# Kernel optimization log

Measured on AMD Instinct MI355X. Metric: run time of the kernel, lower is better.

## Reference

```python
import jax, jax.numpy as jnp
import numpy as np

D = 256      # dim
H = 8        # num_heads
HD = D // H  # head dim
P = 256      # patch_size
B = 4        # num clouds
L = 32768    # points per cloud (divisible by P)
N = B * L
MLP = int(D * 2.0)
PEH = max(32, D // 4)
EPS = 1e-5


def setup_inputs() -> dict:
    key = jax.random.key(0)
    ks = jax.random.split(key, 20)
    s = 0.02
    w = lambda k, shp: jax.random.normal(k, shp, jnp.float32) * s
    inp = {
        "feats": jax.random.normal(ks[0], (N, D), jnp.float32),
        "coord": jax.random.uniform(ks[1], (N, 3), jnp.float32),
        "lengths": jnp.full((B,), L, jnp.int32),
        # CoordPositionalEncoding: Linear(3,PEH) -> ReLU -> Linear(PEH,D)
        "pe_w1": w(ks[2], (3, PEH)), "pe_b1": jnp.zeros((PEH,), jnp.float32),
        "pe_w2": w(ks[3], (PEH, D)), "pe_b2": jnp.zeros((D,), jnp.float32),
        "pre_g": jnp.ones((D,), jnp.float32), "pre_b": jnp.zeros((D,), jnp.float32),
        # block: norm1 + MHA + norm2 + MLP
        "n1_g": jnp.ones((D,), jnp.float32), "n1_b": jnp.zeros((D,), jnp.float32),
        "wqkv": w(ks[4], (D, 3 * D)), "bqkv": jnp.zeros((3 * D,), jnp.float32),
        "wo": w(ks[5], (D, D)), "bo": jnp.zeros((D,), jnp.float32),
        "n2_g": jnp.ones((D,), jnp.float32), "n2_b": jnp.zeros((D,), jnp.float32),
        "m_w1": w(ks[6], (D, MLP)), "m_b1": jnp.zeros((MLP,), jnp.float32),
        "m_w2": w(ks[7], (MLP, D)), "m_b2": jnp.zeros((D,), jnp.float32),
        # global_gate: Linear(2D,D)->ReLU->Linear(D,D)->Sigmoid
        "gg_w1": w(ks[8], (2 * D, D)), "gg_b1": jnp.zeros((D,), jnp.float32),
        "gg_w2": w(ks[9], (D, D)), "gg_b2": jnp.zeros((D,), jnp.float32),
        # fuse: Linear(2D,D)->ReLU->Linear(D,D)
        "f_w1": w(ks[10], (2 * D, D)), "f_b1": jnp.zeros((D,), jnp.float32),
        "f_w2": w(ks[11], (D, D)), "f_b2": jnp.zeros((D,), jnp.float32),
    }
    return inp


def _ln(x, g, b):
    m = x.mean(-1, keepdims=True)
    v = jnp.mean((x - m) ** 2, -1, keepdims=True)
    return (x - m) * jax.lax.rsqrt(v + EPS) * g + b


def _sgca(feats, coord, lengths,
          pe_w1, pe_b1, pe_w2, pe_b2, pre_g, pre_b,
          n1_g, n1_b, wqkv, bqkv, wo, bo, n2_g, n2_b,
          m_w1, m_b1, m_w2, m_b2,
          gg_w1, gg_b1, gg_w2, gg_b2, f_w1, f_b1, f_w2, f_b2):
    Bn = lengths.shape[0]
    Ln = feats.shape[0] // Bn  # equal-length clouds

    def cloud(f, c):  # f: [L, D], c: [L, 3]
        # positional encoding (per-cloud centered / max-abs scaled coords)
        cc = c - c.mean(0, keepdims=True)
        scale = jnp.clip(jnp.abs(cc).max(0, keepdims=True), 1e-6)
        pe = jax.nn.relu((cc / scale) @ pe_w1 + pe_b1) @ pe_w2 + pe_b2
        x = _ln(f + pe, pre_g, pre_b)
        # serialization order from min-max normalized coords
        cn = c - c.min(0, keepdims=True)
        cn = cn / jnp.clip(cn.max(0, keepdims=True), 1e-6)
        key = cn[:, 0] + 2.17 * cn[:, 1] + 3.31 * cn[:, 2]
        order = jnp.argsort(key)
        xs = x[order].reshape(-1, P, D)  # [NP, P, D] block-diagonal windows
        # attention block (pre-norm MHA + residual)
        h = _ln(xs, n1_g, n1_b)
        qkv = h @ wqkv + bqkv
        q = qkv[..., :D].reshape(-1, P, H, HD)
        k = qkv[..., D:2 * D].reshape(-1, P, H, HD)
        v = qkv[..., 2 * D:].reshape(-1, P, H, HD)
        scores = jnp.einsum('nphd,nqhd->nhpq', q, k) / np.sqrt(HD).astype(np.float32)
        a = jax.nn.softmax(scores, axis=-1)
        o = jnp.einsum('nhpq,nqhd->nphd', a, v).reshape(-1, P, D)
        xs = xs + (o @ wo + bo)
        # MLP + residual
        xs = xs + (jax.nn.gelu(_ln(xs, n2_g, n2_b) @ m_w1 + m_b1, approximate=False) @ m_w2 + m_b2)
        # undo serialization
        xo = xs.reshape(-1, D)[jnp.argsort(order)]
        # global token gate/fuse
        gt = jnp.broadcast_to(xo.mean(0, keepdims=True), xo.shape)
        gate = jax.nn.sigmoid(jax.nn.relu(jnp.concatenate([f, gt], -1) @ gg_w1 + gg_b1) @ gg_w2 + gg_b2)
        fused = jax.nn.relu(jnp.concatenate([xo, gt], -1) @ f_w1 + f_b1) @ f_w2 + f_b2
        return f + gate * fused

    out = jax.vmap(cloud)(feats.reshape(Bn, Ln, D), coord.reshape(Bn, Ln, 3))
    return out.reshape(-1, D)


def reference(feats, coord, lengths,
              pe_w1, pe_b1, pe_w2, pe_b2, pre_g, pre_b,
              n1_g, n1_b, wqkv, bqkv, wo, bo, n2_g, n2_b,
              m_w1, m_b1, m_w2, m_b2,
              gg_w1, gg_b1, gg_w2, gg_b2, f_w1, f_b1, f_w2, f_b2):
    return _sgca(feats, coord, lengths,
                 pe_w1, pe_b1, pe_w2, pe_b2, pre_g, pre_b,
                 n1_g, n1_b, wqkv, bqkv, wo, bo, n2_g, n2_b,
                 m_w1, m_b1, m_w2, m_b2,
                 gg_w1, gg_b1, gg_w2, gg_b2, f_w1, f_b1, f_w2, f_b2)
```

## Files before the change

### kernel.cpp

```cpp
#include <hip/hip_runtime.h>
#include <hip/hip_bf16.h>
#include <math.h>

#define D_DIM 256
#define NHEAD 8
#define HDIM 32
#define PATCH 256
#define NCLOUD 4
#define LPC 32768
#define NTOT (NCLOUD * LPC)
#define MLPD 512
#define PEHID 64
#define LN_EPS 1e-5f
#define NCHUNK 4
#define CROWS (NTOT / NCHUNK)

typedef unsigned long long u64;
typedef unsigned short u16;
typedef short bf16x8 __attribute__((ext_vector_type(8)));
typedef float f32x4 __attribute__((ext_vector_type(4)));

__device__ __forceinline__ u16 f2bf(float x) {
  unsigned u = __float_as_uint(x);
  u += 0x7fffu + ((u >> 16) & 1u);
  return (u16)(u >> 16);
}
__device__ __forceinline__ float bf2f(u16 u) {
  return __uint_as_float(((unsigned)u) << 16);
}

__device__ __forceinline__ void gload_lds16(const u16* g, u16* l) {
  __builtin_amdgcn_global_load_lds((const __attribute__((address_space(1))) void*)g,
                                   (__attribute__((address_space(3))) void*)l, 16, 0, 0);
}

__global__ __launch_bounds__(256) void stats_kernel(const float* __restrict__ coord,
                                                    float* __restrict__ stats) {
  const int c = blockIdx.x, t = threadIdx.x;
  float sm[3] = {0.f, 0.f, 0.f};
  float mn[3] = {1e30f, 1e30f, 1e30f};
  float mx[3] = {-1e30f, -1e30f, -1e30f};
  const float* cp = coord + (size_t)c * LPC * 3;
  for (int i = t; i < LPC; i += 256) {
#pragma unroll
    for (int a = 0; a < 3; a++) {
      float v = cp[(size_t)i * 3 + a];
      sm[a] += v;
      mn[a] = fminf(mn[a], v);
      mx[a] = fmaxf(mx[a], v);
    }
  }
  __shared__ float sb[256];
  float rsum[3], rmn[3], rmx[3];
#pragma unroll
  for (int a = 0; a < 3; a++) {
    sb[t] = sm[a]; __syncthreads();
    for (int s = 128; s > 0; s >>= 1) { if (t < s) sb[t] += sb[t + s]; __syncthreads(); }
    rsum[a] = sb[0]; __syncthreads();
    sb[t] = mn[a]; __syncthreads();
    for (int s = 128; s > 0; s >>= 1) { if (t < s) sb[t] = fminf(sb[t], sb[t + s]); __syncthreads(); }
    rmn[a] = sb[0]; __syncthreads();
    sb[t] = mx[a]; __syncthreads();
    for (int s = 128; s > 0; s >>= 1) { if (t < s) sb[t] = fmaxf(sb[t], sb[t + s]); __syncthreads(); }
    rmx[a] = sb[0]; __syncthreads();
  }
  if (t == 0) {
    float* st = stats + c * 16;
#pragma unroll
    for (int a = 0; a < 3; a++) {
      float mean = rsum[a] / (float)LPC;
      st[a] = mean;
      st[3 + a] = fmaxf(fmaxf(rmx[a] - mean, mean - rmn[a]), 1e-6f);
      st[6 + a] = rmn[a];
      st[9 + a] = fmaxf(rmx[a] - rmn[a], 1e-6f);
    }
  }
}

__global__ __launch_bounds__(256) void key_kernel(const float* __restrict__ coord,
                                                  const float* __restrict__ stats,
                                                  u64* __restrict__ keys) {
#pragma clang fp contract(off)
  const int g = blockIdx.x * 256 + threadIdx.x;
  const int c = g >> 15;
  const float* st = stats + c * 16;
  float k0 = (coord[(size_t)g * 3 + 0] - st[6]) / st[9];
  float k1 = (coord[(size_t)g * 3 + 1] - st[7]) / st[10];
  float k2 = (coord[(size_t)g * 3 + 2] - st[8]) / st[11];
  float key = k0 + 2.17f * k1;
  key = key + 3.31f * k2;
  keys[g] = ((u64)__float_as_uint(key) << 32) | (unsigned)(g & (LPC - 1));
}

__global__ __launch_bounds__(1024) void sort_local_kernel(u64* __restrict__ keys) {
  __shared__ u64 s[4096];
  const int base = blockIdx.x * 4096;
  const int t = threadIdx.x;
  for (int i = t; i < 4096; i += 1024) s[i] = keys[base + i];
  __syncthreads();
  for (int k = 2; k <= 4096; k <<= 1) {
    for (int j = k >> 1; j > 0; j >>= 1) {
      for (int p = t; p < 2048; p += 1024) {
        int i = ((p & ~(j - 1)) << 1) | (p & (j - 1));
        int l = i | j;
        bool asc = (((base + i) & (LPC - 1)) & k) == 0;
        u64 a = s[i], bb = s[l];
        if (asc ? (a > bb) : (a < bb)) { s[i] = bb; s[l] = a; }
      }
      __syncthreads();
    }
  }
  for (int i = t; i < 4096; i += 1024) keys[base + i] = s[i];
}

__global__ __launch_bounds__(256) void sort_global_kernel(u64* __restrict__ keys, int k, int j) {
  int p = blockIdx.x * 256 + threadIdx.x;
  int i = ((p & ~(j - 1)) << 1) | (p & (j - 1));
  int l = i | j;
  bool asc = ((i & (LPC - 1)) & k) == 0;
  u64 a = keys[i], b = keys[l];
  if (asc ? (a > b) : (a < b)) { keys[i] = b; keys[l] = a; }
}

__global__ __launch_bounds__(1024) void sort_finish_kernel(u64* __restrict__ keys, int k) {
  __shared__ u64 s[4096];
  const int base = blockIdx.x * 4096;
  const int t = threadIdx.x;
  for (int i = t; i < 4096; i += 1024) s[i] = keys[base + i];
  __syncthreads();
  for (int j = 2048; j > 0; j >>= 1) {
    for (int p = t; p < 2048; p += 1024) {
      int i = ((p & ~(j - 1)) << 1) | (p & (j - 1));
      int l = i | j;
      bool asc = (((base + i) & (LPC - 1)) & k) == 0;
      u64 a = s[i], bb = s[l];
      if (asc ? (a > bb) : (a < bb)) { s[i] = bb; s[l] = a; }
    }
    __syncthreads();
  }
  for (int i = t; i < 4096; i += 1024) keys[base + i] = s[i];
}

__global__ __launch_bounds__(256) void rank_kernel(const u64* __restrict__ keys,
                                                   int* __restrict__ order,
                                                   int* __restrict__ rank) {
  const int g = blockIdx.x * 256 + threadIdx.x;
  const int src = (int)(unsigned)(keys[g] & 0xffffffffULL) + (g & ~(LPC - 1));
  order[g] = src;
  rank[src] = g;
}

__global__ __launch_bounds__(256) void wtrans_kernel(const float* __restrict__ src,
                                                     u16* __restrict__ dst, int R, int C) {
  __shared__ float t[32][33];
  const int bx = blockIdx.x * 32, by = blockIdx.y * 32;
  const int lc = threadIdx.x & 31, lr = threadIdx.x >> 5;
  for (int i = 0; i < 32; i += 8) t[lr + i][lc] = src[(size_t)(by + lr + i) * C + bx + lc];
  __syncthreads();
  for (int i = 0; i < 32; i += 8)
    dst[(size_t)(bx + lr + i) * R + by + lc] = f2bf(t[lc][lr + i]);
}

__global__ __launch_bounds__(256) void conv_bf16_kernel(const float* __restrict__ in,
                                                        u16* __restrict__ out) {
  size_t i = ((size_t)blockIdx.x * 256 + threadIdx.x) * 4;
  float4 v = *(const float4*)(in + i);
  ushort4 o;
  o.x = f2bf(v.x); o.y = f2bf(v.y); o.z = f2bf(v.z); o.w = f2bf(v.w);
  *(ushort4*)(out + i) = o;
}

__global__ __launch_bounds__(256) void h_kernel(const float* __restrict__ coord,
                                                const float* __restrict__ stats,
                                                const float* __restrict__ pw1,
                                                const float* __restrict__ pb1,
                                                u16* __restrict__ H) {
  const int idx = blockIdx.x * 256 + threadIdx.x;
  const int row = idx >> 6, j = idx & 63;
  const int c = row >> 15;
  const float* st = stats + c * 16;
  float s0 = (coord[(size_t)row * 3 + 0] - st[0]) / st[3];
  float s1 = (coord[(size_t)row * 3 + 1] - st[1]) / st[4];
  float s2 = (coord[(size_t)row * 3 + 2] - st[2]) / st[5];
  float h = pb1[j] + s0 * pw1[j] + s1 * pw1[64 + j] + s2 * pw1[128 + j];
  H[idx] = f2bf(fmaxf(h, 0.f));
}

__global__ __launch_bounds__(256) void add_ln_kernel(const float* __restrict__ feats,
                                                     const u16* __restrict__ pe,
                                                     const int* __restrict__ rank,
                                                     const float* __restrict__ g,
                                                     const float* __restrict__ b,
                                                     float* __restrict__ xs) {
  const int row = blockIdx.x * 4 + (threadIdx.x >> 6);
  const int lane = threadIdx.x & 63;
  float4 f = *(const float4*)(feats + (size_t)row * 256 + lane * 4);
  ushort4 p = *(const ushort4*)(pe + (size_t)row * 256 + lane * 4);
  float v0 = f.x + bf2f(p.x), v1 = f.y + bf2f(p.y);
  float v2 = f.z + bf2f(p.z), v3 = f.w + bf2f(p.w);
  float s = v0 + v1 + v2 + v3;
#pragma unroll
  for (int o = 32; o > 0; o >>= 1) s += __shfl_xor(s, o);
  float mean = s * (1.f / 256.f);
  float d0 = v0 - mean, d1 = v1 - mean, d2 = v2 - mean, d3 = v3 - mean;
  float ss = d0 * d0 + d1 * d1 + d2 * d2 + d3 * d3;
#pragma unroll
  for (int o = 32; o > 0; o >>= 1) ss += __shfl_xor(ss, o);
  float inv = 1.f / sqrtf(ss * (1.f / 256.f) + LN_EPS);
  float4 gv = *(const float4*)(g + lane * 4);
  float4 bv = *(const float4*)(b + lane * 4);
  int dst = rank[row];
  float4 o4;
  o4.x = d0 * inv * gv.x + bv.x; o4.y = d1 * inv * gv.y + bv.y;
  o4.z = d2 * inv * gv.z + bv.z; o4.w = d3 * inv * gv.w + bv.w;
  *(float4*)(xs + (size_t)dst * 256 + lane * 4) = o4;
}

__global__ __launch_bounds__(256) void ln_bf16_kernel(const float* __restrict__ in,
                                                      const float* __restrict__ g,
                                                      const float* __restrict__ b,
                                                      u16* __restrict__ out) {
  const int row = blockIdx.x * 4 + (threadIdx.x >> 6);
  const int lane = threadIdx.x & 63;
  float4 v = *(const float4*)(in + (size_t)row * 256 + lane * 4);
  float s = v.x + v.y + v.z + v.w;
#pragma unroll
  for (int o = 32; o > 0; o >>= 1) s += __shfl_xor(s, o);
  float mean = s * (1.f / 256.f);
  float d0 = v.x - mean, d1 = v.y - mean, d2 = v.z - mean, d3 = v.w - mean;
  float ss = d0 * d0 + d1 * d1 + d2 * d2 + d3 * d3;
#pragma unroll
  for (int o = 32; o > 0; o >>= 1) ss += __shfl_xor(ss, o);
  float inv = 1.f / sqrtf(ss * (1.f / 256.f) + LN_EPS);
  float4 gv = *(const float4*)(g + lane * 4);
  float4 bv = *(const float4*)(b + lane * 4);
  ushort4 o4;
  o4.x = f2bf(d0 * inv * gv.x + bv.x); o4.y = f2bf(d1 * inv * gv.y + bv.y);
  o4.z = f2bf(d2 * inv * gv.z + bv.z); o4.w = f2bf(d3 * inv * gv.w + bv.w);
  *(ushort4*)(out + (size_t)row * 256 + lane * 4) = o4;
}

__global__ __launch_bounds__(256) void scatter_bf16_kernel(const int* __restrict__ order,
                                                           const float* __restrict__ xs,
                                                           u16* __restrict__ xo) {
  const int row = blockIdx.x * 4 + (threadIdx.x >> 6);
  const int lane = threadIdx.x & 63;
  float4 v = *(const float4*)(xs + (size_t)row * 256 + lane * 4);
  const int dst = order[row];
  ushort4 o;
  o.x = f2bf(v.x); o.y = f2bf(v.y); o.z = f2bf(v.z); o.w = f2bf(v.w);
  *(ushort4*)(xo + (size_t)dst * 256 + lane * 4) = o;
}

template <int K, int ACT, int MODE, bool EXTRA>
__global__ __launch_bounds__(256, 4) void mfma_gemm(const u16* __restrict__ A,
                                                    const u16* __restrict__ Wt,
                                                    const float* __restrict__ bias,
                                                    const float* __restrict__ extra,
                                                    void* __restrict__ Cout, int Ko) {
  __shared__ __align__(16) u16 Al[128 * 32];
  __shared__ __align__(16) u16 Bl[128 * 32];
  const int tid = threadIdx.x;
  const int lane = tid & 63, wave = tid >> 6;
  const int wr = wave >> 1, wc = wave & 1;
  const int l15 = lane & 15, l4 = lane >> 4;
  const size_t row0 = (size_t)blockIdx.y * 128;
  const int col0 = blockIdx.x * 128;
  const int q0 = wave * 64 + lane;
  const int q1 = q0 + 256;
  const u16* gA0 = A + (row0 + (q0 >> 2)) * K + (q0 & 3) * 8;
  const u16* gA1 = A + (row0 + (q1 >> 2)) * K + (q1 & 3) * 8;
  const u16* gB0 = Wt + (size_t)(col0 + (q0 >> 2)) * K + (q0 & 3) * 8;
  const u16* gB1 = Wt + (size_t)(col0 + (q1 >> 2)) * K + (q1 & 3) * 8;
  u16* lA0 = Al + wave * 512;
  u16* lA1 = Al + 2048 + wave * 512;
  u16* lB0 = Bl + wave * 512;
  u16* lB1 = Bl + 2048 + wave * 512;
  f32x4 acc[4][4];
#pragma unroll
  for (int i = 0; i < 4; i++)
#pragma unroll
    for (int j = 0; j < 4; j++) acc[i][j] = f32x4{0.f, 0.f, 0.f, 0.f};
#pragma unroll 1
  for (int k0 = 0; k0 < K; k0 += 32) {
    gload_lds16(gA0 + k0, lA0);
    gload_lds16(gA1 + k0, lA1);
    gload_lds16(gB0 + k0, lB0);
    gload_lds16(gB1 + k0, lB1);
    __syncthreads();
    bf16x8 af[4], bfr[4];
#pragma unroll
    for (int rb = 0; rb < 4; rb++)
      af[rb] = *(const bf16x8*)&Al[(wr * 64 + rb * 16 + l15) * 32 + l4 * 8];
#pragma unroll
    for (int cb = 0; cb < 4; cb++)
      bfr[cb] = *(const bf16x8*)&Bl[(wc * 64 + cb * 16 + l15) * 32 + l4 * 8];
#pragma unroll
    for (int rb = 0; rb < 4; rb++)
#pragma unroll
      for (int cb = 0; cb < 4; cb++)
        acc[rb][cb] = __builtin_amdgcn_mfma_f32_16x16x32_bf16(af[rb], bfr[cb], acc[rb][cb], 0, 0, 0);
    __syncthreads();
  }
#pragma unroll
  for (int rb = 0; rb < 4; rb++)
#pragma unroll
    for (int cb = 0; cb < 4; cb++)
#pragma unroll
      for (int r = 0; r < 4; r++) {
        size_t row = row0 + wr * 64 + rb * 16 + l4 * 4 + r;
        int col = col0 + wc * 64 + cb * 16 + l15;
        float v = acc[rb][cb][r] + bias[col];
        if (EXTRA) v += extra[((int)(row >> 15)) * 256 + col];
        if (ACT == 1) v = fmaxf(v, 0.f);
        else if (ACT == 2) v = 0.5f * v * (1.f + erff(v * 0.70710678118654752440f));
        else if (ACT == 3) v = 1.f / (1.f + __expf(-v));
        size_t o = row * (size_t)Ko + col;
        if (MODE == 0) ((float*)Cout)[o] = v;
        else if (MODE == 1) ((float*)Cout)[o] += v;
        else ((u16*)Cout)[o] = f2bf(v);
      }
}

__global__ __launch_bounds__(256, 2) void fuse2_kernel(const u16* __restrict__ A1,
                                                       const u16* __restrict__ A2,
                                                       const u16* __restrict__ B1t,
                                                       const u16* __restrict__ B2t,
                                                       const float* __restrict__ bias1,
                                                       const float* __restrict__ bias2,
                                                       const float* __restrict__ feats,
                                                       float* __restrict__ out) {
  __shared__ __align__(16) u16 A1l[128 * 32];
  __shared__ __align__(16) u16 A2l[128 * 32];
  __shared__ __align__(16) u16 B1l[128 * 32];
  __shared__ __align__(16) u16 B2l[128 * 32];
  const int tid = threadIdx.x;
  const int lane = tid & 63, wave = tid >> 6;
  const int wr = wave >> 1, wc = wave & 1;
  const int l15 = lane & 15, l4 = lane >> 4;
  const size_t row0 = (size_t)blockIdx.y * 128;
  const int col0 = blockIdx.x * 128;
  const int q0 = wave * 64 + lane;
  const int q1 = q0 + 256;
  const size_t a0off = (row0 + (q0 >> 2)) * 256 + (q0 & 3) * 8;
  const size_t a1off = (row0 + (q1 >> 2)) * 256 + (q1 & 3) * 8;
  const size_t b0off = (size_t)(col0 + (q0 >> 2)) * 256 + (q0 & 3) * 8;
  const size_t b1off = (size_t)(col0 + (q1 >> 2)) * 256 + (q1 & 3) * 8;
  f32x4 acc1[4][4], acc2[4][4];
#pragma unroll
  for (int i = 0; i < 4; i++)
#pragma unroll
    for (int j = 0; j < 4; j++) {
      acc1[i][j] = f32x4{0.f, 0.f, 0.f, 0.f};
      acc2[i][j] = f32x4{0.f, 0.f, 0.f, 0.f};
    }
#pragma unroll 1
  for (int k0 = 0; k0 < 256; k0 += 32) {
    gload_lds16(A1 + a0off + k0, A1l + wave * 512);
    gload_lds16(A1 + a1off + k0, A1l + 2048 + wave * 512);
    gload_lds16(A2 + a0off + k0, A2l + wave * 512);
    gload_lds16(A2 + a1off + k0, A2l + 2048 + wave * 512);
    gload_lds16(B1t + b0off + k0, B1l + wave * 512);
    gload_lds16(B1t + b1off + k0, B1l + 2048 + wave * 512);
    gload_lds16(B2t + b0off + k0, B2l + wave * 512);
    gload_lds16(B2t + b1off + k0, B2l + 2048 + wave * 512);
    __syncthreads();
#pragma unroll
    for (int rb = 0; rb < 4; rb++) {
      bf16x8 a1f = *(const bf16x8*)&A1l[(wr * 64 + rb * 16 + l15) * 32 + l4 * 8];
      bf16x8 a2f = *(const bf16x8*)&A2l[(wr * 64 + rb * 16 + l15) * 32 + l4 * 8];
#pragma unroll
      for (int cb = 0; cb < 4; cb++) {
        bf16x8 b1f = *(const bf16x8*)&B1l[(wc * 64 + cb * 16 + l15) * 32 + l4 * 8];
        bf16x8 b2f = *(const bf16x8*)&B2l[(wc * 64 + cb * 16 + l15) * 32 + l4 * 8];
        acc1[rb][cb] = __builtin_amdgcn_mfma_f32_16x16x32_bf16(a1f, b1f, acc1[rb][cb], 0, 0, 0);
        acc2[rb][cb] = __builtin_amdgcn_mfma_f32_16x16x32_bf16(a2f, b2f, acc2[rb][cb], 0, 0, 0);
      }
    }
    __syncthreads();
  }
#pragma unroll
  for (int rb = 0; rb < 4; rb++)
#pragma unroll
    for (int cb = 0; cb < 4; cb++)
#pragma unroll
      for (int r = 0; r < 4; r++) {
        size_t row = row0 + wr * 64 + rb * 16 + l4 * 4 + r;
        int col = col0 + wc * 64 + cb * 16 + l15;
        float g = 1.f / (1.f + __expf(-(acc1[rb][cb][r] + bias1[col])));
        float fv = acc2[rb][cb][r] + bias2[col];
        size_t o = row * 256 + col;
        out[o] = feats[o] + g * fv;
      }
}

__global__ __launch_bounds__(256, 3) void attn_mfma_kernel(const u16* __restrict__ qkv,
                                                           u16* __restrict__ ao) {
  __shared__ __align__(16) u16 VT[32 * 264];
  __shared__ __align__(16) u16 Pl[4][16 * 264];
  const int w = blockIdx.x, h = blockIdx.y;
  const int tid = threadIdx.x;
  const int lane = tid & 63, wave = tid >> 6;
  const int l15 = lane & 15, l4 = lane >> 4;
  const size_t base = (size_t)w * PATCH;
  {
    const u16* vrow = qkv + (base + tid) * 768 + 512 + h * HDIM;
#pragma unroll
    for (int d4 = 0; d4 < 8; d4++) {
      ushort4 v4 = *(const ushort4*)(vrow + d4 * 4);
      VT[(d4 * 4 + 0) * 264 + tid] = v4.x;
      VT[(d4 * 4 + 1) * 264 + tid] = v4.y;
      VT[(d4 * 4 + 2) * 264 + tid] = v4.z;
      VT[(d4 * 4 + 3) * 264 + tid] = v4.w;
    }
  }
  __syncthreads();
  u16* Pw = &Pl[wave][0];
  const float scale = 0.17677669529663687f;
  const f32x4 zero = {0.f, 0.f, 0.f, 0.f};
  for (int qt = 0; qt < 4; qt++) {
    const int qbase = wave * 64 + qt * 16;
    bf16x8 qf = *(const bf16x8*)(qkv + (base + qbase + l15) * 768 + h * HDIM + l4 * 8);
    f32x4 s[16];
#pragma unroll
    for (int kt = 0; kt < 16; kt++) {
      bf16x8 kf = *(const bf16x8*)(qkv + (base + kt * 16 + l15) * 768 + 256 + h * HDIM + l4 * 8);
      s[kt] = __builtin_amdgcn_mfma_f32_16x16x32_bf16(kf, qf, zero, 0, 0, 0);
    }
    float m = -1e30f;
#pragma unroll
    for (int kt = 0; kt < 16; kt++)
#pragma unroll
      for (int r = 0; r < 4; r++) { s[kt][r] *= scale; m = fmaxf(m, s[kt][r]); }
    m = fmaxf(m, __shfl_xor(m, 16));
    m = fmaxf(m, __shfl_xor(m, 32));
    float lsum = 0.f;
#pragma unroll
    for (int kt = 0; kt < 16; kt++) {
      float p0 = __expf(s[kt][0] - m), p1 = __expf(s[kt][1] - m);
      float p2 = __expf(s[kt][2] - m), p3 = __expf(s[kt][3] - m);
      lsum += (p0 + p1) + (p2 + p3);
      ushort4 pw4;
      pw4.x = f2bf(p0); pw4.y = f2bf(p1); pw4.z = f2bf(p2); pw4.w = f2bf(p3);
      *(ushort4*)&Pw[l15 * 264 + kt * 16 + l4 * 4] = pw4;
    }
    lsum += __shfl_xor(lsum, 16);
    lsum += __shfl_xor(lsum, 32);
    f32x4 o0 = zero, o1 = zero;
#pragma unroll
    for (int kc = 0; kc < 8; kc++) {
      bf16x8 pf = *(const bf16x8*)&Pw[l15 * 264 + kc * 32 + l4 * 8];
      bf16x8 va = *(const bf16x8*)&VT[l15 * 264 + kc * 32 + l4 * 8];
      bf16x8 vb = *(const bf16x8*)&VT[(16 + l15) * 264 + kc * 32 + l4 * 8];
      o0 = __builtin_amdgcn_mfma_f32_16x16x32_bf16(va, pf, o0, 0, 0, 0);
      o1 = __builtin_amdgcn_mfma_f32_16x16x32_bf16(vb, pf, o1, 0, 0, 0);
    }
    float inv = 1.f / lsum;
    u16* op = ao + (base + qbase + l15) * D_DIM + h * HDIM;
    ushort4 w0, w1;
    w0.x = f2bf(o0[0] * inv); w0.y = f2bf(o0[1] * inv);
    w0.z = f2bf(o0[2] * inv); w0.w = f2bf(o0[3] * inv);
    w1.x = f2bf(o1[0] * inv); w1.y = f2bf(o1[1] * inv);
    w1.z = f2bf(o1[2] * inv); w1.w = f2bf(o1[3] * inv);
    *(ushort4*)(op + l4 * 4) = w0;
    *(ushort4*)(op + 16 + l4 * 4) = w1;
  }
}

__global__ __launch_bounds__(256) void gt_partial_kernel(const float* __restrict__ xs,
                                                         float* __restrict__ part) {
  const int s = blockIdx.x, c = blockIdx.y;
  const int t = threadIdx.x;
  float acc = 0.f;
  const size_t base = (size_t)c * LPC + (size_t)s * 256;
  for (int r = 0; r < 256; r++) acc += xs[(base + r) * D_DIM + t];
  part[(size_t)(c * 128 + s) * D_DIM + t] = acc;
}

__global__ __launch_bounds__(256) void gt_reduce_kernel(const float* __restrict__ part,
                                                        float* __restrict__ gt) {
  const int c = blockIdx.x, t = threadIdx.x;
  float s = 0.f;
  for (int i = 0; i < 128; i++) s += part[(size_t)(c * 128 + i) * D_DIM + t];
  gt[c * D_DIM + t] = s * (1.f / (float)LPC);
}

__global__ __launch_bounds__(256) void pervec_kernel(const float* __restrict__ gt,
                                                     const float* __restrict__ ggw1,
                                                     const float* __restrict__ fw1,
                                                     float* __restrict__ ggt,
                                                     float* __restrict__ fgt) {
  const int c = blockIdx.x, which = blockIdx.y;
  const int t = threadIdx.x;
  const float* W = which ? fw1 : ggw1;
  float* o = which ? fgt : ggt;
  __shared__ float g[D_DIM];
  g[t] = gt[c * D_DIM + t];
  __syncthreads();
  float acc = 0.f;
#pragma unroll 8
  for (int k = 0; k < D_DIM; k++) acc += g[k] * W[(size_t)(256 + k) * D_DIM + t];
  o[c * D_DIM + t] = acc;
}

extern "C" void kernel_launch(void* const* d_in, const int* in_sizes, int n_in,
                              void* d_out, int out_size, void* d_ws, size_t ws_size,
                              hipStream_t stream) {
  const float* feats = (const float*)d_in[0];
  const float* coord = (const float*)d_in[1];
  const float* pe_w1 = (const float*)d_in[3];
  const float* pe_b1 = (const float*)d_in[4];
  const float* pe_w2 = (const float*)d_in[5];
  const float* pe_b2 = (const float*)d_in[6];
  const float* pre_g = (const float*)d_in[7];
  const float* pre_b = (const float*)d_in[8];
  const float* n1_g = (const float*)d_in[9];
  const float* n1_b = (const float*)d_in[10];
  const float* wqkv = (const float*)d_in[11];
  const float* bqkv = (const float*)d_in[12];
  const float* wo = (const float*)d_in[13];
  const float* bo = (const float*)d_in[14];
  const float* n2_g = (const float*)d_in[15];
  const float* n2_b = (const float*)d_in[16];
  const float* m_w1 = (const float*)d_in[17];
  const float* m_b1 = (const float*)d_in[18];
  const float* m_w2 = (const float*)d_in[19];
  const float* m_b2 = (const float*)d_in[20];
  const float* gg_w1 = (const float*)d_in[21];
  const float* gg_b1 = (const float*)d_in[22];
  const float* gg_w2 = (const float*)d_in[23];
  const float* gg_b2 = (const float*)d_in[24];
  const float* f_w1 = (const float*)d_in[25];
  const float* f_b1 = (const float*)d_in[26];
  const float* f_w2 = (const float*)d_in[27];
  const float* f_b2 = (const float*)d_in[28];
  float* out = (float*)d_out;

  char* ws = (char*)d_ws;
  float* xs = (float*)(ws);
  u16* hbuf = (u16*)(ws + 134217728);
  u16* qkvchunk = (u16*)(ws + 201326592);
  u16* aochunk = (u16*)(ws + 251658240);
  u16* tbuf = (u16*)(ws + 268435456);
  u16* Hbuf = (u16*)(ws + 268435456);
  u16* xobf = (u16*)(ws + 201326592);
  size_t off = 301989888;
  u64* keybuf = (u64*)(ws + off); off += (size_t)NTOT * 8;
  int* orderbuf = (int*)(ws + off); off += (size_t)NTOT * 4;
  int* rankbuf = (int*)(ws + off); off += (size_t)NTOT * 4;
  float* statsbuf = (float*)(ws + off); off += 4096;
  float* gtpart = (float*)(ws + off); off += (size_t)NCLOUD * 128 * D_DIM * 4;
  float* gtbuf = (float*)(ws + off); off += 4096;
  float* ggtbuf = (float*)(ws + off); off += 4096;
  float* fgtbuf = (float*)(ws + off); off += 4096;
  u16* wqkvT = (u16*)(ws + off); off += 768 * 256 * 2;
  u16* woT = (u16*)(ws + off); off += 256 * 256 * 2;
  u16* mw1T = (u16*)(ws + off); off += 512 * 256 * 2;
  u16* mw2T = (u16*)(ws + off); off += 256 * 512 * 2;
  u16* ggw1T = (u16*)(ws + off); off += 256 * 256 * 2;
  u16* ggw2T = (u16*)(ws + off); off += 256 * 256 * 2;
  u16* fw1T = (u16*)(ws + off); off += 256 * 256 * 2;
  u16* fw2T = (u16*)(ws + off); off += 256 * 256 * 2;
  u16* pw2T = (u16*)(ws + off); off += 64 * 256 * 2;
  u16* featsbf = (u16*)(ws);
  u16* u1buf = (u16*)(ws + 67108864);

  stats_kernel<<<NCLOUD, 256, 0, stream>>>(coord, statsbuf);
  key_kernel<<<NTOT / 256, 256, 0, stream>>>(coord, statsbuf, keybuf);
  sort_local_kernel<<<NTOT / 4096, 1024, 0, stream>>>(keybuf);
  for (int k = 8192; k <= 32768; k <<= 1) {
    for (int j = k >> 1; j >= 4096; j >>= 1)
      sort_global_kernel<<<NTOT / 512, 256, 0, stream>>>(keybuf, k, j);
    sort_finish_kernel<<<NTOT / 4096, 1024, 0, stream>>>(keybuf, k);
  }
  rank_kernel<<<NTOT / 256, 256, 0, stream>>>(keybuf, orderbuf, rankbuf);
  wtrans_kernel<<<dim3(24, 8), 256, 0, stream>>>(wqkv, wqkvT, 256, 768);
  wtrans_kernel<<<dim3(8, 8), 256, 0, stream>>>(wo, woT, 256, 256);
  wtrans_kernel<<<dim3(16, 8), 256, 0, stream>>>(m_w1, mw1T, 256, 512);
  wtrans_kernel<<<dim3(8, 16), 256, 0, stream>>>(m_w2, mw2T, 512, 256);
  wtrans_kernel<<<dim3(8, 8), 256, 0, stream>>>(gg_w1, ggw1T, 256, 256);
  wtrans_kernel<<<dim3(8, 8), 256, 0, stream>>>(gg_w2, ggw2T, 256, 256);
  wtrans_kernel<<<dim3(8, 8), 256, 0, stream>>>(f_w1, fw1T, 256, 256);
  wtrans_kernel<<<dim3(8, 8), 256, 0, stream>>>(f_w2, fw2T, 256, 256);
  wtrans_kernel<<<dim3(8, 2), 256, 0, stream>>>(pe_w2, pw2T, 64, 256);
  h_kernel<<<NTOT * 64 / 256, 256, 0, stream>>>(coord, statsbuf, pe_w1, pe_b1, Hbuf);
  mfma_gemm<64, 0, 2, false><<<dim3(2, NTOT / 128), 256, 0, stream>>>(
      Hbuf, pw2T, pe_b2, nullptr, hbuf, 256);
  add_ln_kernel<<<NTOT / 4, 256, 0, stream>>>(feats, hbuf, rankbuf, pre_g, pre_b, xs);
  ln_bf16_kernel<<<NTOT / 4, 256, 0, stream>>>(xs, n1_g, n1_b, hbuf);
  for (int ch = 0; ch < NCHUNK; ch++) {
    const size_t ro = (size_t)ch * CROWS;
    mfma_gemm<256, 0, 2, false><<<dim3(6, CROWS / 128), 256, 0, stream>>>(
        hbuf + ro * 256, wqkvT, bqkv, nullptr, qkvchunk, 768);
    attn_mfma_kernel<<<dim3(CROWS / PATCH, NHEAD), 256, 0, stream>>>(qkvchunk, aochunk);
    mfma_gemm<256, 0, 1, false><<<dim3(2, CROWS / 128), 256, 0, stream>>>(
        aochunk, woT, bo, nullptr, xs + ro * 256, 256);
  }
  ln_bf16_kernel<<<NTOT / 4, 256, 0, stream>>>(xs, n2_g, n2_b, hbuf);
  for (int ch = 0; ch < NCHUNK; ch++) {
    const size_t ro = (size_t)ch * CROWS;
    mfma_gemm<256, 2, 2, false><<<dim3(MLPD / 128, CROWS / 128), 256, 0, stream>>>(
        hbuf + ro * 256, mw1T, m_b1, nullptr, tbuf, 512);
    mfma_gemm<512, 0, 1, false><<<dim3(2, CROWS / 128), 256, 0, stream>>>(
        tbuf, mw2T, m_b2, nullptr, xs + ro * 256, 256);
  }
  scatter_bf16_kernel<<<NTOT / 4, 256, 0, stream>>>(orderbuf, xs, xobf);
  gt_partial_kernel<<<dim3(128, NCLOUD), 256, 0, stream>>>(xs, gtpart);
  gt_reduce_kernel<<<NCLOUD, 256, 0, stream>>>(gtpart, gtbuf);
  pervec_kernel<<<dim3(NCLOUD, 2), 256, 0, stream>>>(gtbuf, gg_w1, f_w1, ggtbuf, fgtbuf);
  conv_bf16_kernel<<<NTOT * 256 / 1024, 256, 0, stream>>>(feats, featsbf);
  mfma_gemm<256, 1, 2, true><<<dim3(2, NTOT / 128), 256, 0, stream>>>(
      featsbf, ggw1T, gg_b1, ggtbuf, hbuf, 256);
  mfma_gemm<256, 1, 2, true><<<dim3(2, NTOT / 128), 256, 0, stream>>>(
      xobf, fw1T, f_b1, fgtbuf, u1buf, 256);
  fuse2_kernel<<<dim3(2, NTOT / 128), 256, 0, stream>>>(
      hbuf, u1buf, ggw2T, fw2T, gg_b2, f_b2, feats, out);
  (void)in_sizes; (void)n_in; (void)out_size; (void)ws_size;
}
```

Before: 1.422 ms.

## Fuse residual GEMMs with LayerNorm and scatter epilogues; retile fuse2 kernel

Adds a full-row GEMM kernel (64 rows by all 256 output columns per block) that adds the residual and bias into xs. For the output projection it also computes LayerNorm2 in the epilogue and writes bf16, which removes the separate ln_bf16 pass. For the second MLP GEMM it scatters the bf16 result by the serialization order, which removes scatter_bf16_kernel. fuse2 is retiled to 64-column tiles with more blocks and occupancy 3, trading fewer separate memory passes for larger per-block B tiles and reductions through LDS.

```diff
diff --git a/kernel.cpp b/kernel.cpp
--- a/kernel.cpp
+++ b/kernel.cpp
@@ -238,18 +238,6 @@
   o4.x = f2bf(d0 * inv * gv.x + bv.x); o4.y = f2bf(d1 * inv * gv.y + bv.y);
   o4.z = f2bf(d2 * inv * gv.z + bv.z); o4.w = f2bf(d3 * inv * gv.w + bv.w);
   *(ushort4*)(out + (size_t)row * 256 + lane * 4) = o4;
-}
-
-__global__ __launch_bounds__(256) void scatter_bf16_kernel(const int* __restrict__ order,
-                                                           const float* __restrict__ xs,
-                                                           u16* __restrict__ xo) {
-  const int row = blockIdx.x * 4 + (threadIdx.x >> 6);
-  const int lane = threadIdx.x & 63;
-  float4 v = *(const float4*)(xs + (size_t)row * 256 + lane * 4);
-  const int dst = order[row];
-  ushort4 o;
-  o.x = f2bf(v.x); o.y = f2bf(v.y); o.z = f2bf(v.z); o.w = f2bf(v.w);
-  *(ushort4*)(xo + (size_t)dst * 256 + lane * 4) = o;
 }
 
 template <int K, int ACT, int MODE, bool EXTRA>
@@ -322,7 +310,146 @@
       }
 }
 
-__global__ __launch_bounds__(256, 2) void fuse2_kernel(const u16* __restrict__ A1,
+template <int K, int EPI>
+__global__ __launch_bounds__(256, 3) void mfma_row_gemm(const u16* __restrict__ A,
+                                                        const u16* __restrict__ Wt,
+                                                        const float* __restrict__ bias,
+                                                        float* __restrict__ xs,
+                                                        u16* __restrict__ hout,
+                                                        const int* __restrict__ order,
+                                                        const float* __restrict__ g,
+                                                        const float* __restrict__ b) {
+  __shared__ __align__(16) u16 Al[64 * 32];
+  __shared__ __align__(16) u16 Bl[256 * 32];
+  __shared__ float reds[2][4][64];
+  const int tid = threadIdx.x;
+  const int lane = tid & 63, wave = tid >> 6;
+  const int l15 = lane & 15, l4 = lane >> 4;
+  const size_t row0 = (size_t)blockIdx.x * 64;
+  const u16* gA = A + (row0 + (tid >> 2)) * K + (tid & 3) * 8;
+  u16* lA = Al + wave * 512;
+  const u16* gB[4];
+  u16* lB[4];
+#pragma unroll
+  for (int s = 0; s < 4; s++) {
+    int q = s * 256 + tid;
+    gB[s] = Wt + (size_t)(q >> 2) * K + (q & 3) * 8;
+    lB[s] = Bl + s * 2048 + wave * 512;
+  }
+  f32x4 acc[4][4];
+#pragma unroll
+  for (int i = 0; i < 4; i++)
+#pragma unroll
+    for (int j = 0; j < 4; j++) acc[i][j] = f32x4{0.f, 0.f, 0.f, 0.f};
+#pragma unroll 1
+  for (int k0 = 0; k0 < K; k0 += 32) {
+    gload_lds16(gA + k0, lA);
+#pragma unroll
+    for (int s = 0; s < 4; s++) gload_lds16(gB[s] + k0, lB[s]);
+    __syncthreads();
+    bf16x8 af[4], bfr[4];
+#pragma unroll
+    for (int rb = 0; rb < 4; rb++)
+      af[rb] = *(const bf16x8*)&Al[(rb * 16 + l15) * 32 + l4 * 8];
+#pragma unroll
+    for (int cb = 0; cb < 4; cb++)
+      bfr[cb] = *(const bf16x8*)&Bl[(wave * 64 + cb * 16 + l15) * 32 + l4 * 8];
+#pragma unroll
+    for (int rb = 0; rb < 4; rb++)
+#pragma unroll
+      for (int cb = 0; cb < 4; cb++)
+        acc[rb][cb] = __builtin_amdgcn_mfma_f32_16x16x32_bf16(af[rb], bfr[cb], acc[rb][cb], 0, 0, 0);
+    __syncthreads();
+  }
+#pragma unroll
+  for (int rb = 0; rb < 4; rb++)
+#pragma unroll
+    for (int cb = 0; cb < 4; cb++)
+#pragma unroll
+      for (int r = 0; r < 4; r++) {
+        size_t row = row0 + rb * 16 + l4 * 4 + r;
+        int col = wave * 64 + cb * 16 + l15;
+        size_t o = row * 256 + col;
+        float t = xs[o] + acc[rb][cb][r] + bias[col];
+        xs[o] = t;
+        acc[rb][cb][r] = t;
+      }
+  if (EPI == 1) {
+    float ps[4][4];
+#pragma unroll
+    for (int rb = 0; rb < 4; rb++)
+#pragma unroll
+      for (int r = 0; r < 4; r++) {
+        float v = acc[rb][0][r] + acc[rb][1][r] + acc[rb][2][r] + acc[rb][3][r];
+#pragma unroll
+        for (int oo = 1; oo < 16; oo <<= 1) v += __shfl_xor(v, oo);
+        ps[rb][r] = v;
+      }
+    if (l15 == 0)
+#pragma unroll
+      for (int rb = 0; rb < 4; rb++)
+#pragma unroll
+        for (int r = 0; r < 4; r++) reds[0][wave][rb * 16 + l4 * 4 + r] = ps[rb][r];
+    __syncthreads();
+    float mean[4][4];
+#pragma unroll
+    for (int rb = 0; rb < 4; rb++)
+#pragma unroll
+      for (int r = 0; r < 4; r++) {
+        int ri = rb * 16 + l4 * 4 + r;
+        mean[rb][r] = (reds[0][0][ri] + reds[0][1][ri] + reds[0][2][ri] + reds[0][3][ri]) *
+                      (1.f / 256.f);
+      }
+#pragma unroll
+    for (int rb = 0; rb < 4; rb++)
+#pragma unroll
+      for (int r = 0; r < 4; r++) {
+        float d0 = acc[rb][0][r] - mean[rb][r], d1 = acc[rb][1][r] - mean[rb][r];
+        float d2 = acc[rb][2][r] - mean[rb][r], d3 = acc[rb][3][r] - mean[rb][r];
+        float v = d0 * d0 + d1 * d1 + d2 * d2 + d3 * d3;
+#pragma unroll
+        for (int oo = 1; oo < 16; oo <<= 1) v += __shfl_xor(v, oo);
+        ps[rb][r] = v;
+      }
+    if (l15 == 0)
+#pragma unroll
+      for (int rb = 0; rb < 4; rb++)
+#pragma unroll
+        for (int r = 0; r < 4; r++) reds[1][wave][rb * 16 + l4 * 4 + r] = ps[rb][r];
+    __syncthreads();
+#pragma unroll
+    for (int rb = 0; rb < 4; rb++)
+#pragma unroll
+      for (int r = 0; r < 4; r++) {
+        int ri = rb * 16 + l4 * 4 + r;
+        float var = (reds[1][0][ri] + reds[1][1][ri] + reds[1][2][ri] + reds[1][3][ri]) *
+                    (1.f / 256.f);
+        float inv = 1.f / sqrtf(var + LN_EPS);
+        size_t row = row0 + ri;
+#pragma unroll
+        for (int cb = 0; cb < 4; cb++) {
+          int col = wave * 64 + cb * 16 + l15;
+          hout[row * 256 + col] =
+              f2bf((acc[rb][cb][r] - mean[rb][r]) * inv * g[col] + b[col]);
+        }
+      }
+  } else {
+#pragma unroll
+    for (int rb = 0; rb < 4; rb++)
+#pragma unroll
+      for (int r = 0; r < 4; r++) {
+        size_t row = row0 + rb * 16 + l4 * 4 + r;
+        size_t dst = (size_t)order[row];
+#pragma unroll
+        for (int cb = 0; cb < 4; cb++) {
+          int col = wave * 64 + cb * 16 + l15;
+          hout[dst * 256 + col] = f2bf(acc[rb][cb][r]);
+        }
+      }
+  }
+}
+
+__global__ __launch_bounds__(256, 3) void fuse2_kernel(const u16* __restrict__ A1,
                                                        const u16* __restrict__ A2,
                                                        const u16* __restrict__ B1t,
                                                        const u16* __restrict__ B2t,
@@ -332,23 +459,20 @@
                                                        float* __restrict__ out) {
   __shared__ __align__(16) u16 A1l[128 * 32];
   __shared__ __align__(16) u16 A2l[128 * 32];
-  __shared__ __align__(16) u16 B1l[128 * 32];
-  __shared__ __align__(16) u16 B2l[128 * 32];
+  __shared__ __align__(16) u16 B1l[64 * 32];
+  __shared__ __align__(16) u16 B2l[64 * 32];
   const int tid = threadIdx.x;
   const int lane = tid & 63, wave = tid >> 6;
-  const int wr = wave >> 1, wc = wave & 1;
   const int l15 = lane & 15, l4 = lane >> 4;
   const size_t row0 = (size_t)blockIdx.y * 128;
-  const int col0 = blockIdx.x * 128;
-  const int q0 = wave * 64 + lane;
-  const int q1 = q0 + 256;
+  const int col0 = blockIdx.x * 64;
+  const int q0 = tid, q1 = tid + 256;
   const size_t a0off = (row0 + (q0 >> 2)) * 256 + (q0 & 3) * 8;
   const size_t a1off = (row0 + (q1 >> 2)) * 256 + (q1 & 3) * 8;
-  const size_t b0off = (size_t)(col0 + (q0 >> 2)) * 256 + (q0 & 3) * 8;
-  const size_t b1off = (size_t)(col0 + (q1 >> 2)) * 256 + (q1 & 3) * 8;
-  f32x4 acc1[4][4], acc2[4][4];
-#pragma unroll
-  for (int i = 0; i < 4; i++)
+  const size_t boff = (size_t)(col0 + (q0 >> 2)) * 256 + (q0 & 3) * 8;
+  f32x4 acc1[2][4], acc2[2][4];
+#pragma unroll
+  for (int i = 0; i < 2; i++)
 #pragma unroll
     for (int j = 0; j < 4; j++) {
       acc1[i][j] = f32x4{0.f, 0.f, 0.f, 0.f};
@@ -360,19 +484,17 @@
     gload_lds16(A1 + a1off + k0, A1l + 2048 + wave * 512);
     gload_lds16(A2 + a0off + k0, A2l + wave * 512);
     gload_lds16(A2 + a1off + k0, A2l + 2048 + wave * 512);
-    gload_lds16(B1t + b0off + k0, B1l + wave * 512);
-    gload_lds16(B1t + b1off + k0, B1l + 2048 + wave * 512);
-    gload_lds16(B2t + b0off + k0, B2l + wave * 512);
-    gload_lds16(B2t + b1off + k0, B2l + 2048 + wave * 512);
-    __syncthreads();
-#pragma unroll
-    for (int rb = 0; rb < 4; rb++) {
-      bf16x8 a1f = *(const bf16x8*)&A1l[(wr * 64 + rb * 16 + l15) * 32 + l4 * 8];
-      bf16x8 a2f = *(const bf16x8*)&A2l[(wr * 64 + rb * 16 + l15) * 32 + l4 * 8];
+    gload_lds16(B1t + boff + k0, B1l + wave * 512);
+    gload_lds16(B2t + boff + k0, B2l + wave * 512);
+    __syncthreads();
+#pragma unroll
+    for (int rb = 0; rb < 2; rb++) {
+      bf16x8 a1f = *(const bf16x8*)&A1l[(wave * 32 + rb * 16 + l15) * 32 + l4 * 8];
+      bf16x8 a2f = *(const bf16x8*)&A2l[(wave * 32 + rb * 16 + l15) * 32 + l4 * 8];
 #pragma unroll
       for (int cb = 0; cb < 4; cb++) {
-        bf16x8 b1f = *(const bf16x8*)&B1l[(wc * 64 + cb * 16 + l15) * 32 + l4 * 8];
-        bf16x8 b2f = *(const bf16x8*)&B2l[(wc * 64 + cb * 16 + l15) * 32 + l4 * 8];
+        bf16x8 b1f = *(const bf16x8*)&B1l[(cb * 16 + l15) * 32 + l4 * 8];
+        bf16x8 b2f = *(const bf16x8*)&B2l[(cb * 16 + l15) * 32 + l4 * 8];
         acc1[rb][cb] = __builtin_amdgcn_mfma_f32_16x16x32_bf16(a1f, b1f, acc1[rb][cb], 0, 0, 0);
         acc2[rb][cb] = __builtin_amdgcn_mfma_f32_16x16x32_bf16(a2f, b2f, acc2[rb][cb], 0, 0, 0);
       }
@@ -380,17 +502,17 @@
     __syncthreads();
   }
 #pragma unroll
-  for (int rb = 0; rb < 4; rb++)
+  for (int rb = 0; rb < 2; rb++)
 #pragma unroll
     for (int cb = 0; cb < 4; cb++)
 #pragma unroll
       for (int r = 0; r < 4; r++) {
-        size_t row = row0 + wr * 64 + rb * 16 + l4 * 4 + r;
-        int col = col0 + wc * 64 + cb * 16 + l15;
-        float g = 1.f / (1.f + __expf(-(acc1[rb][cb][r] + bias1[col])));
+        size_t row = row0 + wave * 32 + rb * 16 + l4 * 4 + r;
+        int col = col0 + cb * 16 + l15;
+        float gg = 1.f / (1.f + __expf(-(acc1[rb][cb][r] + bias1[col])));
         float fv = acc2[rb][cb][r] + bias2[col];
         size_t o = row * 256 + col;
-        out[o] = feats[o] + g * fv;
+        out[o] = feats[o] + gg * fv;
       }
 }
 
@@ -593,18 +715,16 @@
     mfma_gemm<256, 0, 2, false><<<dim3(6, CROWS / 128), 256, 0, stream>>>(
         hbuf + ro * 256, wqkvT, bqkv, nullptr, qkvchunk, 768);
     attn_mfma_kernel<<<dim3(CROWS / PATCH, NHEAD), 256, 0, stream>>>(qkvchunk, aochunk);
-    mfma_gemm<256, 0, 1, false><<<dim3(2, CROWS / 128), 256, 0, stream>>>(
-        aochunk, woT, bo, nullptr, xs + ro * 256, 256);
-  }
-  ln_bf16_kernel<<<NTOT / 4, 256, 0, stream>>>(xs, n2_g, n2_b, hbuf);
+    mfma_row_gemm<256, 1><<<CROWS / 64, 256, 0, stream>>>(
+        aochunk, woT, bo, xs + ro * 256, hbuf + ro * 256, nullptr, n2_g, n2_b);
+  }
   for (int ch = 0; ch < NCHUNK; ch++) {
     const size_t ro = (size_t)ch * CROWS;
     mfma_gemm<256, 2, 2, false><<<dim3(MLPD / 128, CROWS / 128), 256, 0, stream>>>(
         hbuf + ro * 256, mw1T, m_b1, nullptr, tbuf, 512);
-    mfma_gemm<512, 0, 1, false><<<dim3(2, CROWS / 128), 256, 0, stream>>>(
-        tbuf, mw2T, m_b2, nullptr, xs + ro * 256, 256);
-  }
-  scatter_bf16_kernel<<<NTOT / 4, 256, 0, stream>>>(orderbuf, xs, xobf);
+    mfma_row_gemm<512, 2><<<CROWS / 64, 256, 0, stream>>>(
+        tbuf, mw2T, m_b2, xs + ro * 256, xobf, orderbuf + ro, nullptr, nullptr);
+  }
   gt_partial_kernel<<<dim3(128, NCLOUD), 256, 0, stream>>>(xs, gtpart);
   gt_reduce_kernel<<<NCLOUD, 256, 0, stream>>>(gtpart, gtbuf);
   pervec_kernel<<<dim3(NCLOUD, 2), 256, 0, stream>>>(gtbuf, gg_w1, f_w1, ggtbuf, fgtbuf);
@@ -613,7 +733,7 @@
       featsbf, ggw1T, gg_b1, ggtbuf, hbuf, 256);
   mfma_gemm<256, 1, 2, true><<<dim3(2, NTOT / 128), 256, 0, stream>>>(
       xobf, fw1T, f_b1, fgtbuf, u1buf, 256);
-  fuse2_kernel<<<dim3(2, NTOT / 128), 256, 0, stream>>>(
+  fuse2_kernel<<<dim3(4, NTOT / 128), 256, 0, stream>>>(
       hbuf, u1buf, ggw2T, fw2T, gg_b2, f_b2, feats, out);
   (void)in_sizes; (void)n_in; (void)out_size; (void)ws_size;
 }
```

New measurement: 1.398 ms. About the same (-1.7%).
